# Kernel tuning notes

Hardware: AMD Instinct MI355X
Metric: run time of the kernel (lower is better)

The kernel has to match this reference:

```python
import jax, jax.numpy as jnp
import numpy as np

B, T, D = 2, 2048, 1024
QH, KVH = 16, 4
HD = D // QH          # 64
G = QH // KVH         # group size 4
SCALE = HD ** -0.5


def _rope_rotate(x):
    # interleaved rotation: (x1, x2) -> (-x2, x1)
    x1 = x[..., ::2]
    x2 = x[..., 1::2]
    return jnp.stack((-x2, x1), axis=-1).reshape(x.shape)


def setup_inputs() -> dict:
    key = jax.random.key(0)
    k0, k1, k2, k3 = jax.random.split(key, 4)
    x = jax.random.normal(k0, (B, T, D), dtype=jnp.float32)
    # proper RoPE tables, shape [T, HD], each frequency repeated for the interleaved pair
    inv_freq = 1.0 / (10000.0 ** (np.arange(0, HD, 2, dtype=np.float32) / HD))
    freqs = np.arange(T, dtype=np.float32)[:, None] * inv_freq[None, :]   # [T, HD/2]
    freqs = np.repeat(freqs, 2, axis=-1)                                   # [T, HD]
    cos = jnp.asarray(np.cos(freqs), dtype=jnp.float32)
    sin = jnp.asarray(np.sin(freqs), dtype=jnp.float32)
    # glorot-uniform weights stored torch-style as [out, in]
    def glorot(k, out_d, in_d):
        lim = float(np.sqrt(6.0 / (in_d + out_d)))
        return jax.random.uniform(k, (out_d, in_d), jnp.float32, -lim, lim)
    Wq = glorot(k1, D, D)
    Wkv = glorot(k2, 2 * KVH * HD, D)
    Wo = glorot(k3, D, D)
    return {"x": x, "cos": cos, "sin": sin, "Wq": Wq, "Wkv": Wkv, "Wo": Wo}


def reference(x, cos, sin, Wq, Wkv, Wo):
    # projections (torch Linear: y = x @ W.T)
    q = (x @ Wq.T).reshape(B, T, QH, HD).transpose(0, 2, 1, 3)        # [B,QH,T,HD]
    kv = (x @ Wkv.T).reshape(B, T, KVH, 2, HD)
    k = kv[..., 0, :].transpose(0, 2, 1, 3)                            # [B,KVH,T,HD]
    v = kv[..., 1, :].transpose(0, 2, 1, 3)                            # [B,KVH,T,HD]
    # inline RoPE (cos/sin broadcast over batch & heads)
    q = q * cos + _rope_rotate(q) * sin
    k = k * cos + _rope_rotate(k) * sin
    # GQA via broadcast instead of repeat_interleave (same math)
    qg = q.reshape(B, KVH, G, T, HD)
    scores = jnp.einsum('bkgtd,bksd->bkgts', qg, k) * SCALE            # [B,KVH,G,T,T]
    attn = jax.nn.softmax(scores, axis=-1)  # dropout is identity in eval
    out = jnp.einsum('bkgts,bksd->bkgtd', attn, v)                     # [B,KVH,G,T,HD]
    out = out.reshape(B, QH, T, HD).transpose(0, 2, 1, 3).reshape(B, T, D)
    return out @ Wo.T
```

## Files before the change

### kernel.cpp

```cpp
#include <hip/hip_runtime.h>


typedef __bf16 bf16x8 __attribute__((ext_vector_type(8)));
typedef float f32x4 __attribute__((ext_vector_type(4)));
typedef float f32x16 __attribute__((ext_vector_type(16)));
typedef int i32x4 __attribute__((ext_vector_type(4)));
typedef unsigned short ushort4v __attribute__((ext_vector_type(4)));
typedef unsigned short ushort8v __attribute__((ext_vector_type(8)));
typedef unsigned short u16;
typedef unsigned int u32;

#define DEVINL __device__ __forceinline__

DEVINL float bf2f(u16 u) {
  unsigned int x = ((unsigned int)u) << 16;
  return __builtin_bit_cast(float, x);
}
DEVINL u16 f2bf(float f) {
  unsigned int x = __builtin_bit_cast(unsigned int, f);
  x += 0x7fffu + ((x >> 16) & 1u);
  return (u16)(x >> 16);
}
DEVINL float exp2r(float x) {
  float r;
  asm("v_exp_f32 %0, %1" : "=v"(r) : "v"(x));
  return r;
}
DEVINL void gld16(const u16* g, u16* l) {
  __builtin_amdgcn_global_load_lds(
      (const __attribute__((address_space(1))) void*)g,
      (__attribute__((address_space(3))) void*)l, 16, 0, 0);
}

constexpr int Bb = 2, Tt = 2048, Dd = 1024, QH = 16, KVH = 4, HD = 64;
constexpr float SCALE_L2E = 0.125f * 1.44269504088896340736f;
constexpr int KVSZ = 131072;

__global__ void cvt_all(const float* __restrict__ x, const float* __restrict__ Wq,
                        const float* __restrict__ Wkv, const float* __restrict__ Wo,
                        u16* __restrict__ xb, u16* __restrict__ wqkv,
                        u16* __restrict__ wob) {
  int i = blockIdx.x * 256 + threadIdx.x;
  const float* src;
  u16* dst;
  if (i < 1048576) {
    src = x; dst = xb;
  } else if (i < 1310720) {
    src = Wq - (size_t)1048576 * 4; dst = wqkv - (size_t)1048576 * 4;
  } else if (i < 1441792) {
    src = Wkv - (size_t)1310720 * 4; dst = wqkv + (size_t)1024 * 1024 - (size_t)1310720 * 4;
  } else {
    src = Wo - (size_t)1441792 * 4; dst = wob - (size_t)1441792 * 4;
  }
  float4 v = reinterpret_cast<const float4*>(src)[i];
  ushort4v o = {f2bf(v.x), f2bf(v.y), f2bf(v.z), f2bf(v.w)};
  *reinterpret_cast<ushort4v*>(dst + (size_t)i * 4) = o;
}

template <bool OUT_F32, int BNF>
__global__ __launch_bounds__(256) void gemm_bt(const u16* __restrict__ A,
                                               const u16* __restrict__ Bw,
                                               void* __restrict__ Cout, int M, int N, int K) {
  __shared__ alignas(16) u16 lA[128 * 64];
  __shared__ alignas(16) u16 lB[BNF * 32 * 64];
  const int tid = threadIdx.x;
  const int w = tid >> 6, lane = tid & 63;
  const int r16 = lane & 15, g4 = lane >> 4;
  const int row0 = blockIdx.y * 128, col0 = blockIdx.x * (BNF * 32);
  const int sr = tid >> 3, sc = tid & 7;
  const int NT = K >> 6;

  bf16x8 ra[4], rb[BNF];
  f32x4 acc[4][BNF];
#pragma unroll
  for (int i = 0; i < 4; ++i)
#pragma unroll
    for (int j = 0; j < BNF; ++j) acc[i][j] = f32x4{0.f, 0.f, 0.f, 0.f};

  const int wm = (w >> 1) * 64, wn = (w & 1) * (BNF * 8);

#pragma unroll
  for (int i = 0; i < 4; ++i) {
    int r = i * 32 + sr;
    ra[i] = *reinterpret_cast<const bf16x8*>(A + (size_t)(row0 + r) * K + sc * 8);
  }
#pragma unroll
  for (int i = 0; i < BNF; ++i) {
    int r = i * 32 + sr;
    rb[i] = *reinterpret_cast<const bf16x8*>(Bw + (size_t)(col0 + r) * K + sc * 8);
  }

  for (int kt = 0; kt < NT; ++kt) {
    __syncthreads();
#pragma unroll
    for (int i = 0; i < 4; ++i) {
      int r = i * 32 + sr;
      int c = (sc ^ (r & 7)) * 8;
      *reinterpret_cast<bf16x8*>(&lA[r * 64 + c]) = ra[i];
    }
#pragma unroll
    for (int i = 0; i < BNF; ++i) {
      int r = i * 32 + sr;
      int c = (sc ^ (r & 7)) * 8;
      *reinterpret_cast<bf16x8*>(&lB[r * 64 + c]) = rb[i];
    }
    __syncthreads();
    if (kt + 1 < NT) {
      int k0 = (kt + 1) << 6;
#pragma unroll
      for (int i = 0; i < 4; ++i) {
        int r = i * 32 + sr;
        ra[i] = *reinterpret_cast<const bf16x8*>(A + (size_t)(row0 + r) * K + k0 + sc * 8);
      }
#pragma unroll
      for (int i = 0; i < BNF; ++i) {
        int r = i * 32 + sr;
        rb[i] = *reinterpret_cast<const bf16x8*>(Bw + (size_t)(col0 + r) * K + k0 + sc * 8);
      }
    }
#pragma unroll
    for (int kk = 0; kk < 2; ++kk) {
      bf16x8 af[4], bfr[BNF];
#pragma unroll
      for (int mf = 0; mf < 4; ++mf) {
        int r = wm + mf * 16 + r16;
        int c = ((kk * 4 + g4) ^ (r & 7)) * 8;
        af[mf] = *reinterpret_cast<const bf16x8*>(&lA[r * 64 + c]);
      }
#pragma unroll
      for (int nf = 0; nf < BNF; ++nf) {
        int r = wn * 2 + nf * 16 + r16;
        int c = ((kk * 4 + g4) ^ (r & 7)) * 8;
        bfr[nf] = *reinterpret_cast<const bf16x8*>(&lB[r * 64 + c]);
      }
#pragma unroll
      for (int mf = 0; mf < 4; ++mf)
#pragma unroll
        for (int nf = 0; nf < BNF; ++nf)
          acc[mf][nf] =
              __builtin_amdgcn_mfma_f32_16x16x32_bf16(af[mf], bfr[nf], acc[mf][nf], 0, 0, 0);
    }
  }

#pragma unroll
  for (int mf = 0; mf < 4; ++mf)
#pragma unroll
    for (int nf = 0; nf < BNF; ++nf)
#pragma unroll
      for (int r = 0; r < 4; ++r) {
        size_t row = (size_t)(row0 + wm + mf * 16 + g4 * 4 + r);
        size_t col = (size_t)(col0 + wn * 2 + nf * 16 + r16);
        float v = acc[mf][nf][r];
        if (OUT_F32)
          reinterpret_cast<float*>(Cout)[row * N + col] = v;
        else
          reinterpret_cast<u16*>(Cout)[row * N + col] = f2bf(v);
      }
}

__global__ void rope_vt(const u16* __restrict__ P, const float* __restrict__ cosT,
                        const float* __restrict__ sinT, u16* __restrict__ Q,
                        u16* __restrict__ Kc, u16* __restrict__ Vf) {
  __shared__ u16 tile[64][72];
  const int bid = blockIdx.x;
  const int tid = threadIdx.x;
  if (bid < 10240) {
    int idx = bid * 256 + tid;
    int row = idx / 640, p = idx - row * 640;
    int b = row >> 11, t = row & 2047;
    int n, d;
    u16* outp;
    float scl;
    if (p < 512) {
      n = p * 2;
      int h = n >> 6;
      d = n & 63;
      outp = Q + ((size_t)(b * QH + h) * Tt + t) * HD + d;
      scl = SCALE_L2E;
    } else {
      int r2 = p - 512;
      int kvh = r2 >> 5, dp = r2 & 31;
      d = dp * 2;
      n = 1024 + kvh * 128 + d;
      int bh = b * KVH + kvh;
      int kf = d >> 4, h8 = (d >> 3) & 1, j = d & 7;
      outp = Kc + (size_t)bh * KVSZ + ((t >> 5) * 4 + kf) * 512 + (h8 * 32 + (t & 31)) * 8 + j;
      scl = 1.0f;
    }
    unsigned int pv = *reinterpret_cast<const unsigned int*>(P + (size_t)row * 1536 + n);
    float v0 = bf2f((u16)(pv & 0xffffu)), v1 = bf2f((u16)(pv >> 16));
    float c = cosT[t * HD + d], s = sinT[t * HD + d];
    float o0 = (v0 * c - v1 * s) * scl;
    float o1 = (v1 * c + v0 * s) * scl;
    unsigned int ob = (unsigned int)f2bf(o0) | ((unsigned int)f2bf(o1) << 16);
    *reinterpret_cast<unsigned int*>(outp) = ob;
  } else {
    int rem = bid - 10240;
    int bh = rem >> 5, tt = rem & 31;
    int b = bh >> 2, kvh = bh & 3;
    int t0 = tt * 64;
    int colbase = 1024 + kvh * 128 + 64;
#pragma unroll
    for (int j = 0; j < 4; ++j) {
      int rr = j * 16 + (tid >> 4);
      int cc = (tid & 15) * 4;
      *reinterpret_cast<uint2*>(&tile[rr][cc]) =
          *reinterpret_cast<const uint2*>(P + (size_t)(b * Tt + t0 + rr) * 1536 + colbase + cc);
    }
    __syncthreads();
#pragma unroll
    for (int kk = 0; kk < 2; ++kk) {
      int CH = kk * 256 + tid;
      int df = CH >> 8, sbks = (CH >> 6) & 3, h8 = (CH >> 5) & 1, l = CH & 31;
      int d = df * 32 + l;
      int c = (sbks >> 1) * 4 + (sbks & 1) * 2 + h8;
      ushort8v v;
#pragma unroll
      for (int j = 0; j < 8; ++j) v[j] = tile[c * 8 + j][d];
      u16* dst = Vf + (size_t)bh * KVSZ + (((t0 >> 6) * 2 + df) * 4 + sbks) * 512 +
                 (h8 * 32 + l) * 8;
      *reinterpret_cast<ushort8v*>(dst) = v;
    }
  }
}

__global__ __launch_bounds__(512, 4) void attn_fwd10(const u16* __restrict__ Q,
                                                     const u16* __restrict__ Kf,
                                                     const u16* __restrict__ Vf,
                                                     u16* __restrict__ Oa) {
  __shared__ alignas(16) u16 arena[32768];
  const int tid = threadIdx.x;
  const int w = tid >> 6, lane = tid & 63;
  const int g = w & 3, spl = w >> 2;
  const int l31 = lane & 31, hi = lane >> 5;

  const int fid = blockIdx.x;
  const int xcd = fid & 7, idx = fid >> 3;
  const int b = xcd >> 2, kvh = xcd & 3;
  const int h = kvh * 4 + g;
  const int t0 = idx * 32;
  const size_t bh = (size_t)(b * KVH + kvh);

  const int rg = w & 3;
  const int sv = rg & 1, isV = rg >> 1;
  const u16* gsrc = (isV ? Vf : Kf) + bh * KVSZ + sv * 65536 + spl * 2048 + lane * 8;
  const int ldst0 = isV * 16384 + sv * 4096 + spl * 2048;

  const u16* Qh = Q + ((size_t)(b * QH + h) * Tt + t0 + l31) * HD + hi * 8;
  bf16x8 qf[4];
#pragma unroll
  for (int kf = 0; kf < 4; ++kf)
    qf[kf] = *reinterpret_cast<const bf16x8*>(Qh + kf * 16);

  f32x16 oacc[2];
#pragma unroll
  for (int df = 0; df < 2; ++df)
#pragma unroll
    for (int r = 0; r < 16; ++r) oacc[df][r] = 0.f;
  float lp = 0.f;

#pragma unroll
  for (int i = 0; i < 4; ++i) gld16(gsrc + i * 512, &arena[ldst0 + i * 512]);
  __syncthreads();

  int cur = 0;
  for (int it = 0; it < 16; ++it) {
    if (it < 15) {
      const u16* gs = gsrc + (it + 1) * 4096;
      u16* ld = &arena[ldst0 + (cur ^ 1) * 8192];
#pragma unroll
      for (int i = 0; i < 4; ++i) gld16(gs + i * 512, ld + i * 512);
    }
    const int ktb = cur * 8192 + spl * 4096;
    const int vtb = 16384 + cur * 8192 + spl * 4096;

    f32x16 sacc[2];
#pragma unroll
    for (int sb = 0; sb < 2; ++sb) {
      bf16x8 kfr[4];
#pragma unroll
      for (int kf = 0; kf < 4; ++kf)
        kfr[kf] = *reinterpret_cast<const bf16x8*>(&arena[ktb + sb * 2048 + kf * 512 + lane * 8]);
#pragma unroll
      for (int r = 0; r < 16; ++r) sacc[sb][r] = 0.f;
      __builtin_amdgcn_s_setprio(1);
#pragma unroll
      for (int kf = 0; kf < 4; ++kf)
        sacc[sb] = __builtin_amdgcn_mfma_f32_32x32x16_bf16(kfr[kf], qf[kf], sacc[sb], 0, 0, 0);
      __builtin_amdgcn_s_setprio(0);
    }

    float a0 = 0.f, a1 = 0.f, a2 = 0.f, a3 = 0.f;
#pragma unroll
    for (int sb = 0; sb < 2; ++sb)
#pragma unroll
      for (int r = 0; r < 16; r += 4) {
        float e0 = exp2r(sacc[sb][r]);
        float e1 = exp2r(sacc[sb][r + 1]);
        float e2 = exp2r(sacc[sb][r + 2]);
        float e3 = exp2r(sacc[sb][r + 3]);
        sacc[sb][r] = e0; sacc[sb][r + 1] = e1; sacc[sb][r + 2] = e2; sacc[sb][r + 3] = e3;
        a0 += e0; a1 += e1; a2 += e2; a3 += e3;
      }
    lp += (a0 + a1) + (a2 + a3);

    bf16x8 pf[2][2];
#pragma unroll
    for (int sb = 0; sb < 2; ++sb) {
      u32 pw[8];
#pragma unroll
      for (int r2 = 0; r2 < 8; ++r2) {
        u32 o;
        asm("v_cvt_pk_bf16_f32 %0, %1, %2"
            : "=v"(o)
            : "v"(sacc[sb][2 * r2]), "v"(sacc[sb][2 * r2 + 1]));
        pw[r2] = o;
      }
      u32 fw[2][4];
#pragma unroll
      for (int pp = 0; pp < 4; ++pp) {
        int ks = pp >> 1, o = pp & 1;
        u32 a = pw[ks * 4 + o], bq = pw[ks * 4 + o + 2];
        asm("v_permlane32_swap_b32 %0, %1" : "+v"(a), "+v"(bq));
        fw[ks][o] = a;
        fw[ks][o + 2] = bq;
      }
#pragma unroll
      for (int ks = 0; ks < 2; ++ks) {
        i32x4 iv = {(int)fw[ks][0], (int)fw[ks][1], (int)fw[ks][2], (int)fw[ks][3]};
        pf[sb][ks] = __builtin_bit_cast(bf16x8, iv);
      }
    }

    __builtin_amdgcn_s_setprio(1);
#pragma unroll
    for (int df = 0; df < 2; ++df)
#pragma unroll
      for (int sb = 0; sb < 2; ++sb)
#pragma unroll
        for (int ks = 0; ks < 2; ++ks) {
          bf16x8 vfr = *reinterpret_cast<const bf16x8*>(
              &arena[vtb + (df * 4 + sb * 2 + ks) * 512 + lane * 8]);
          oacc[df] = __builtin_amdgcn_mfma_f32_32x32x16_bf16(vfr, pf[sb][ks], oacc[df], 0, 0, 0);
        }
    __builtin_amdgcn_s_setprio(0);

    __syncthreads();
    cur ^= 1;
  }

  lp += __shfl_xor(lp, 32);
  float* cb = reinterpret_cast<float*>(arena) + ((size_t)g * 32 + l31) * 66;
  if (spl == 1) {
#pragma unroll
    for (int df = 0; df < 2; ++df)
#pragma unroll
      for (int r = 0; r < 16; ++r) {
        int d = df * 32 + (r & 3) + 8 * (r >> 2) + 4 * hi;
        cb[d] = oacc[df][r];
      }
    if (hi == 0) cb[64] = lp;
  }
  __syncthreads();
  if (spl == 0) {
    lp += cb[64];
    float linv = 1.0f / lp;
    u16* otg = arena + 17408 + g * 2304;
#pragma unroll
    for (int df = 0; df < 2; ++df)
#pragma unroll
      for (int r = 0; r < 16; ++r) {
        int d = df * 32 + (r & 3) + 8 * (r >> 2) + 4 * hi;
        otg[l31 * 72 + d] = f2bf((oacc[df][r] + cb[d]) * linv);
      }
  }
  __syncthreads();
  if (spl == 0) {
    const u16* otg = arena + 17408 + g * 2304;
    int tr = lane >> 1, dblk = (lane & 1) * 32;
    u16* gdst = Oa + ((size_t)(b * Tt + t0 + tr)) * Dd + h * HD + dblk;
#pragma unroll
    for (int c = 0; c < 4; ++c) {
      ushort8v vv = *reinterpret_cast<const ushort8v*>(&otg[tr * 72 + dblk + c * 8]);
      *reinterpret_cast<ushort8v*>(gdst + c * 8) = vv;
    }
  }
}

extern "C" void kernel_launch(void* const* d_in, const int* in_sizes, int n_in, void* d_out,
                              int out_size, void* d_ws, size_t ws_size, hipStream_t stream) {
  (void)in_sizes; (void)n_in; (void)out_size; (void)ws_size;
  const float* x = (const float*)d_in[0];
  const float* cosT = (const float*)d_in[1];
  const float* sinT = (const float*)d_in[2];
  const float* Wq = (const float*)d_in[3];
  const float* Wkv = (const float*)d_in[4];
  const float* Wo = (const float*)d_in[5];

  char* p = (char*)d_ws;
  u16* xb = (u16*)p;   p += (size_t)4096 * 1024 * 2;
  u16* wqkv = (u16*)p; p += (size_t)1536 * 1024 * 2;
  u16* wob = (u16*)p;  p += (size_t)1024 * 1024 * 2;
  u16* Pbuf = (u16*)p; p += (size_t)4096 * 1536 * 2;
  u16* Qb = (u16*)p;   p += (size_t)Bb * QH * Tt * HD * 2;
  u16* Kbuf = (u16*)p; p += (size_t)Bb * KVH * Tt * HD * 2;
  u16* Vfb = (u16*)p;  p += (size_t)Bb * KVH * HD * Tt * 2;
  u16* Ob = Pbuf;

  cvt_all<<<6656, 256, 0, stream>>>(x, Wq, Wkv, Wo, xb, wqkv, wob);
  gemm_bt<false, 4><<<dim3(12, 32), 256, 0, stream>>>(xb, wqkv, Pbuf, 4096, 1536, 1024);
  rope_vt<<<10496, 256, 0, stream>>>(Pbuf, cosT, sinT, Qb, Kbuf, Vfb);
  attn_fwd10<<<512, 512, 0, stream>>>(Qb, Kbuf, Vfb, Ob);
  gemm_bt<true, 2><<<dim3(16, 32), 256, 0, stream>>>(Ob, wob, d_out, 4096, 1024, 1024);
}
```

Measured before the change: 99.86 us.

## Double-buffer GEMM LDS tiles with direct global-to-LDS loads

The projection GEMM now stages tiles straight from global memory into a double-buffered LDS area through a gld16 helper, with the XOR swizzle moved onto the global address. The old path loaded into registers and then stored to LDS behind two barriers per step. The next tile is prefetched while the current one is computed, leaving one barrier per iteration. The QKV GEMM also switches to a narrower N tile (BNF 4 to 2) with twice the blocks, which raises block count but lowers per-block reuse and doubles LDS use.

```diff
diff --git a/kernel.cpp b/kernel.cpp
--- a/kernel.cpp
+++ b/kernel.cpp
@@ -61,77 +61,56 @@
 __global__ __launch_bounds__(256) void gemm_bt(const u16* __restrict__ A,
                                                const u16* __restrict__ Bw,
                                                void* __restrict__ Cout, int M, int N, int K) {
-  __shared__ alignas(16) u16 lA[128 * 64];
-  __shared__ alignas(16) u16 lB[BNF * 32 * 64];
+  __shared__ alignas(16) u16 lA[2][128 * 64];
+  __shared__ alignas(16) u16 lB[2][BNF * 32 * 64];
   const int tid = threadIdx.x;
   const int w = tid >> 6, lane = tid & 63;
   const int r16 = lane & 15, g4 = lane >> 4;
   const int row0 = blockIdx.y * 128, col0 = blockIdx.x * (BNF * 32);
   const int sr = tid >> 3, sc = tid & 7;
+  const int csw = sc ^ (sr & 7);
   const int NT = K >> 6;
-
-  bf16x8 ra[4], rb[BNF];
+  const int wm = (w >> 1) * 64, wn2 = (w & 1) * (BNF * 16);
+
   f32x4 acc[4][BNF];
 #pragma unroll
   for (int i = 0; i < 4; ++i)
 #pragma unroll
     for (int j = 0; j < BNF; ++j) acc[i][j] = f32x4{0.f, 0.f, 0.f, 0.f};
 
-  const int wm = (w >> 1) * 64, wn = (w & 1) * (BNF * 8);
-
-#pragma unroll
-  for (int i = 0; i < 4; ++i) {
-    int r = i * 32 + sr;
-    ra[i] = *reinterpret_cast<const bf16x8*>(A + (size_t)(row0 + r) * K + sc * 8);
-  }
-#pragma unroll
-  for (int i = 0; i < BNF; ++i) {
-    int r = i * 32 + sr;
-    rb[i] = *reinterpret_cast<const bf16x8*>(Bw + (size_t)(col0 + r) * K + sc * 8);
-  }
-
+  const u16* Abase = A + (size_t)(row0 + sr) * K + csw * 8;
+  const u16* Bbase = Bw + (size_t)(col0 + sr) * K + csw * 8;
+
+  auto stage = [&](int buf, int kt) {
+    const int k0 = kt << 6;
+#pragma unroll
+    for (int i = 0; i < 4; ++i)
+      gld16(Abase + (size_t)(i * 32) * K + k0, &lA[buf][i * 2048 + w * 512]);
+#pragma unroll
+    for (int i = 0; i < BNF; ++i)
+      gld16(Bbase + (size_t)(i * 32) * K + k0, &lB[buf][i * 2048 + w * 512]);
+  };
+
+  stage(0, 0);
+  __syncthreads();
+
+  int cur = 0;
   for (int kt = 0; kt < NT; ++kt) {
-    __syncthreads();
-#pragma unroll
-    for (int i = 0; i < 4; ++i) {
-      int r = i * 32 + sr;
-      int c = (sc ^ (r & 7)) * 8;
-      *reinterpret_cast<bf16x8*>(&lA[r * 64 + c]) = ra[i];
-    }
-#pragma unroll
-    for (int i = 0; i < BNF; ++i) {
-      int r = i * 32 + sr;
-      int c = (sc ^ (r & 7)) * 8;
-      *reinterpret_cast<bf16x8*>(&lB[r * 64 + c]) = rb[i];
-    }
-    __syncthreads();
-    if (kt + 1 < NT) {
-      int k0 = (kt + 1) << 6;
-#pragma unroll
-      for (int i = 0; i < 4; ++i) {
-        int r = i * 32 + sr;
-        ra[i] = *reinterpret_cast<const bf16x8*>(A + (size_t)(row0 + r) * K + k0 + sc * 8);
-      }
-#pragma unroll
-      for (int i = 0; i < BNF; ++i) {
-        int r = i * 32 + sr;
-        rb[i] = *reinterpret_cast<const bf16x8*>(Bw + (size_t)(col0 + r) * K + k0 + sc * 8);
-      }
-    }
+    if (kt + 1 < NT) stage(cur ^ 1, kt + 1);
 #pragma unroll
     for (int kk = 0; kk < 2; ++kk) {
       bf16x8 af[4], bfr[BNF];
 #pragma unroll
       for (int mf = 0; mf < 4; ++mf) {
         int r = wm + mf * 16 + r16;
-        int c = ((kk * 4 + g4) ^ (r & 7)) * 8;
-        af[mf] = *reinterpret_cast<const bf16x8*>(&lA[r * 64 + c]);
+        int c = (kk * 4 + g4) ^ (r & 7);
+        af[mf] = *reinterpret_cast<const bf16x8*>(&lA[cur][r * 64 + c * 8]);
       }
 #pragma unroll
       for (int nf = 0; nf < BNF; ++nf) {
-        int r = wn * 2 + nf * 16 + r16;
-        int c = ((kk * 4 + g4) ^ (r & 7)) * 8;
-        bfr[nf] = *reinterpret_cast<const bf16x8*>(&lB[r * 64 + c]);
+        int r = wn2 + nf * 16 + r16;
+        int c = (kk * 4 + g4) ^ (r & 7);
+        bfr[nf] = *reinterpret_cast<const bf16x8*>(&lB[cur][r * 64 + c * 8]);
       }
 #pragma unroll
       for (int mf = 0; mf < 4; ++mf)
@@ -140,6 +119,8 @@
           acc[mf][nf] =
               __builtin_amdgcn_mfma_f32_16x16x32_bf16(af[mf], bfr[nf], acc[mf][nf], 0, 0, 0);
     }
+    __syncthreads();
+    cur ^= 1;
   }
 
 #pragma unroll
@@ -149,7 +130,7 @@
 #pragma unroll
       for (int r = 0; r < 4; ++r) {
         size_t row = (size_t)(row0 + wm + mf * 16 + g4 * 4 + r);
-        size_t col = (size_t)(col0 + wn * 2 + nf * 16 + r16);
+        size_t col = (size_t)(col0 + wn2 + nf * 16 + r16);
         float v = acc[mf][nf][r];
         if (OUT_F32)
           reinterpret_cast<float*>(Cout)[row * N + col] = v;
@@ -408,7 +389,7 @@
   u16* Ob = Pbuf;
 
   cvt_all<<<6656, 256, 0, stream>>>(x, Wq, Wkv, Wo, xb, wqkv, wob);
-  gemm_bt<false, 4><<<dim3(12, 32), 256, 0, stream>>>(xb, wqkv, Pbuf, 4096, 1536, 1024);
+  gemm_bt<false, 2><<<dim3(24, 32), 256, 0, stream>>>(xb, wqkv, Pbuf, 4096, 1536, 1024);
   rope_vt<<<10496, 256, 0, stream>>>(Pbuf, cosT, sinT, Qb, Kbuf, Vfb);
   attn_fwd10<<<512, 512, 0, stream>>>(Qb, Kbuf, Vfb, Ob);
   gemm_bt<true, 2><<<dim3(16, 32), 256, 0, stream>>>(Ob, wob, d_out, 4096, 1024, 1024);
```

After: 98.76 us. About the same (-1.1%).

## Fuse RoPE and Q/K/V layout scatter into the QKV projection GEMM epilogue

Applied to the files above, without the earlier changes.

Replaces the separate QKV GEMM plus rope_vt kernel with one GEMM whose epilogue applies RoPE, using a lane shuffle to fetch the paired element, and writes Q, K and the transposed V directly in the attention layouts. This drops the Pbuf round trip through global memory and one kernel launch. The N tile shrinks to 64 columns so each block maps to exactly one head. The trade-off is uncoalesced scattered 2-byte stores and per-element cos/sin loads in the epilogue, and less reuse of A per block.

```diff
diff --git a/kernel.cpp b/kernel.cpp
--- a/kernel.cpp
+++ b/kernel.cpp
@@ -57,6 +57,160 @@
   *reinterpret_cast<ushort4v*>(dst + (size_t)i * 4) = o;
 }
 
+
+__global__ __launch_bounds__(256) void gemm_qkv(const u16* __restrict__ A,
+                                                const u16* __restrict__ Bw,
+                                                const float* __restrict__ cosT,
+                                                const float* __restrict__ sinT,
+                                                u16* __restrict__ Qb,
+                                                u16* __restrict__ Kf,
+                                                u16* __restrict__ Vf) {
+  constexpr int K = 1024;
+  __shared__ alignas(16) u16 lA[128 * 64];
+  __shared__ alignas(16) u16 lB[64 * 64];
+  const int tid = threadIdx.x;
+  const int w = tid >> 6, lane = tid & 63;
+  const int r16 = lane & 15, g4 = lane >> 4;
+  const int row0 = blockIdx.y * 128, col0 = blockIdx.x * 64;
+  const int sr = tid >> 3, sc = tid & 7;
+  const int NT = K >> 6;
+
+  bf16x8 ra[4], rb[2];
+  f32x4 acc[4][2];
+#pragma unroll
+  for (int i = 0; i < 4; ++i)
+#pragma unroll
+    for (int j = 0; j < 2; ++j) acc[i][j] = f32x4{0.f, 0.f, 0.f, 0.f};
+
+  const int wm = (w >> 1) * 64, wn2 = (w & 1) * 32;
+
+#pragma unroll
+  for (int i = 0; i < 4; ++i) {
+    int r = i * 32 + sr;
+    ra[i] = *reinterpret_cast<const bf16x8*>(A + (size_t)(row0 + r) * K + sc * 8);
+  }
+#pragma unroll
+  for (int i = 0; i < 2; ++i) {
+    int r = i * 32 + sr;
+    rb[i] = *reinterpret_cast<const bf16x8*>(Bw + (size_t)(col0 + r) * K + sc * 8);
+  }
+
+  for (int kt = 0; kt < NT; ++kt) {
+    __syncthreads();
+#pragma unroll
+    for (int i = 0; i < 4; ++i) {
+      int r = i * 32 + sr;
+      int c = (sc ^ (r & 7)) * 8;
+      *reinterpret_cast<bf16x8*>(&lA[r * 64 + c]) = ra[i];
+    }
+#pragma unroll
+    for (int i = 0; i < 2; ++i) {
+      int r = i * 32 + sr;
+      int c = (sc ^ (r & 7)) * 8;
+      *reinterpret_cast<bf16x8*>(&lB[r * 64 + c]) = rb[i];
+    }
+    __syncthreads();
+    if (kt + 1 < NT) {
+      int k0 = (kt + 1) << 6;
+#pragma unroll
+      for (int i = 0; i < 4; ++i) {
+        int r = i * 32 + sr;
+        ra[i] = *reinterpret_cast<const bf16x8*>(A + (size_t)(row0 + r) * K + k0 + sc * 8);
+      }
+#pragma unroll
+      for (int i = 0; i < 2; ++i) {
+        int r = i * 32 + sr;
+        rb[i] = *reinterpret_cast<const bf16x8*>(Bw + (size_t)(col0 + r) * K + k0 + sc * 8);
+      }
+    }
+#pragma unroll
+    for (int kk = 0; kk < 2; ++kk) {
+      bf16x8 af[4], bfr[2];
+#pragma unroll
+      for (int mf = 0; mf < 4; ++mf) {
+        int r = wm + mf * 16 + r16;
+        int c = ((kk * 4 + g4) ^ (r & 7)) * 8;
+        af[mf] = *reinterpret_cast<const bf16x8*>(&lA[r * 64 + c]);
+      }
+#pragma unroll
+      for (int nf = 0; nf < 2; ++nf) {
+        int r = wn2 + nf * 16 + r16;
+        int c = ((kk * 4 + g4) ^ (r & 7)) * 8;
+        bfr[nf] = *reinterpret_cast<const bf16x8*>(&lB[r * 64 + c]);
+      }
+#pragma unroll
+      for (int mf = 0; mf < 4; ++mf)
+#pragma unroll
+        for (int nf = 0; nf < 2; ++nf)
+          acc[mf][nf] =
+              __builtin_amdgcn_mfma_f32_16x16x32_bf16(af[mf], bfr[nf], acc[mf][nf], 0, 0, 0);
+    }
+  }
+
+  const float psign = (r16 & 1) ? 1.f : -1.f;
+  if (col0 < 1024) {
+    const int hq = col0 >> 6;
+#pragma unroll
+    for (int nf = 0; nf < 2; ++nf) {
+      const int d = wn2 + nf * 16 + r16;
+#pragma unroll
+      for (int mf = 0; mf < 4; ++mf)
+#pragma unroll
+        for (int r = 0; r < 4; ++r) {
+          int bt = row0 + wm + mf * 16 + g4 * 4 + r;
+          int b = bt >> 11, t = bt & 2047;
+          float v = acc[mf][nf][r];
+          float pv = __shfl_xor(v, 1);
+          float c = cosT[t * 64 + d] * SCALE_L2E;
+          float s = sinT[t * 64 + d] * SCALE_L2E;
+          float o = v * c + psign * pv * s;
+          Qb[((size_t)(b * QH + hq) * Tt + t) * HD + d] = f2bf(o);
+        }
+    }
+  } else {
+    const int kvcol = col0 - 1024;
+    const int kvh = kvcol >> 7, isv = (kvcol >> 6) & 1;
+    if (!isv) {
+#pragma unroll
+      for (int nf = 0; nf < 2; ++nf) {
+        const int d = wn2 + nf * 16 + r16;
+        const int kf = d >> 4, h8 = (d >> 3) & 1, j = d & 7;
+#pragma unroll
+        for (int mf = 0; mf < 4; ++mf)
+#pragma unroll
+          for (int r = 0; r < 4; ++r) {
+            int bt = row0 + wm + mf * 16 + g4 * 4 + r;
+            int b = bt >> 11, t = bt & 2047;
+            float v = acc[mf][nf][r];
+            float pv = __shfl_xor(v, 1);
+            float c = cosT[t * 64 + d], s = sinT[t * 64 + d];
+            float o = v * c + psign * pv * s;
+            size_t bh = (size_t)(b * KVH + kvh);
+            Kf[bh * KVSZ + ((t >> 5) * 4 + kf) * 512 + (h8 * 32 + (t & 31)) * 8 + j] = f2bf(o);
+          }
+      }
+    } else {
+#pragma unroll
+      for (int nf = 0; nf < 2; ++nf) {
+        const int d = wn2 + nf * 16 + r16;
+        const int df = d >> 5, l = d & 31;
+#pragma unroll
+        for (int mf = 0; mf < 4; ++mf)
+#pragma unroll
+          for (int r = 0; r < 4; ++r) {
+            int bt = row0 + wm + mf * 16 + g4 * 4 + r;
+            int b = bt >> 11, t = bt & 2047;
+            size_t bh = (size_t)(b * KVH + kvh);
+            size_t addr = bh * KVSZ +
+                          (((t >> 6) * 2 + df) * 4 + ((t >> 4) & 3)) * 512 +
+                          (((t >> 3) & 1) * 32 + l) * 8 + (t & 7);
+            Vf[addr] = f2bf(acc[mf][nf][r]);
+          }
+      }
+    }
+  }
+}
+
 template <bool OUT_F32, int BNF>
 __global__ __launch_bounds__(256) void gemm_bt(const u16* __restrict__ A,
                                                const u16* __restrict__ Bw,
@@ -77,7 +231,7 @@
 #pragma unroll
     for (int j = 0; j < BNF; ++j) acc[i][j] = f32x4{0.f, 0.f, 0.f, 0.f};
 
-  const int wm = (w >> 1) * 64, wn = (w & 1) * (BNF * 8);
+  const int wm = (w >> 1) * 64, wn2 = (w & 1) * (BNF * 16);
 
 #pragma unroll
   for (int i = 0; i < 4; ++i) {
@@ -129,7 +283,7 @@
       }
 #pragma unroll
       for (int nf = 0; nf < BNF; ++nf) {
-        int r = wn * 2 + nf * 16 + r16;
+        int r = wn2 + nf * 16 + r16;
         int c = ((kk * 4 + g4) ^ (r & 7)) * 8;
         bfr[nf] = *reinterpret_cast<const bf16x8*>(&lB[r * 64 + c]);
       }
@@ -149,79 +303,13 @@
 #pragma unroll
       for (int r = 0; r < 4; ++r) {
         size_t row = (size_t)(row0 + wm + mf * 16 + g4 * 4 + r);
-        size_t col = (size_t)(col0 + wn * 2 + nf * 16 + r16);
+        size_t col = (size_t)(col0 + wn2 + nf * 16 + r16);
         float v = acc[mf][nf][r];
         if (OUT_F32)
           reinterpret_cast<float*>(Cout)[row * N + col] = v;
         else
           reinterpret_cast<u16*>(Cout)[row * N + col] = f2bf(v);
       }
-}
-
-__global__ void rope_vt(const u16* __restrict__ P, const float* __restrict__ cosT,
-                        const float* __restrict__ sinT, u16* __restrict__ Q,
-                        u16* __restrict__ Kc, u16* __restrict__ Vf) {
-  __shared__ u16 tile[64][72];
-  const int bid = blockIdx.x;
-  const int tid = threadIdx.x;
-  if (bid < 10240) {
-    int idx = bid * 256 + tid;
-    int row = idx / 640, p = idx - row * 640;
-    int b = row >> 11, t = row & 2047;
-    int n, d;
-    u16* outp;
-    float scl;
-    if (p < 512) {
-      n = p * 2;
-      int h = n >> 6;
-      d = n & 63;
-      outp = Q + ((size_t)(b * QH + h) * Tt + t) * HD + d;
-      scl = SCALE_L2E;
-    } else {
-      int r2 = p - 512;
-      int kvh = r2 >> 5, dp = r2 & 31;
-      d = dp * 2;
-      n = 1024 + kvh * 128 + d;
-      int bh = b * KVH + kvh;
-      int kf = d >> 4, h8 = (d >> 3) & 1, j = d & 7;
-      outp = Kc + (size_t)bh * KVSZ + ((t >> 5) * 4 + kf) * 512 + (h8 * 32 + (t & 31)) * 8 + j;
-      scl = 1.0f;
-    }
-    unsigned int pv = *reinterpret_cast<const unsigned int*>(P + (size_t)row * 1536 + n);
-    float v0 = bf2f((u16)(pv & 0xffffu)), v1 = bf2f((u16)(pv >> 16));
-    float c = cosT[t * HD + d], s = sinT[t * HD + d];
-    float o0 = (v0 * c - v1 * s) * scl;
-    float o1 = (v1 * c + v0 * s) * scl;
-    unsigned int ob = (unsigned int)f2bf(o0) | ((unsigned int)f2bf(o1) << 16);
-    *reinterpret_cast<unsigned int*>(outp) = ob;
-  } else {
-    int rem = bid - 10240;
-    int bh = rem >> 5, tt = rem & 31;
-    int b = bh >> 2, kvh = bh & 3;
-    int t0 = tt * 64;
-    int colbase = 1024 + kvh * 128 + 64;
-#pragma unroll
-    for (int j = 0; j < 4; ++j) {
-      int rr = j * 16 + (tid >> 4);
-      int cc = (tid & 15) * 4;
-      *reinterpret_cast<uint2*>(&tile[rr][cc]) =
-          *reinterpret_cast<const uint2*>(P + (size_t)(b * Tt + t0 + rr) * 1536 + colbase + cc);
-    }
-    __syncthreads();
-#pragma unroll
-    for (int kk = 0; kk < 2; ++kk) {
-      int CH = kk * 256 + tid;
-      int df = CH >> 8, sbks = (CH >> 6) & 3, h8 = (CH >> 5) & 1, l = CH & 31;
-      int d = df * 32 + l;
-      int c = (sbks >> 1) * 4 + (sbks & 1) * 2 + h8;
-      ushort8v v;
-#pragma unroll
-      for (int j = 0; j < 8; ++j) v[j] = tile[c * 8 + j][d];
-      u16* dst = Vf + (size_t)bh * KVSZ + (((t0 >> 6) * 2 + df) * 4 + sbks) * 512 +
-                 (h8 * 32 + l) * 8;
-      *reinterpret_cast<ushort8v*>(dst) = v;
-    }
-  }
 }
 
 __global__ __launch_bounds__(512, 4) void attn_fwd10(const u16* __restrict__ Q,
@@ -408,8 +496,7 @@
   u16* Ob = Pbuf;
 
   cvt_all<<<6656, 256, 0, stream>>>(x, Wq, Wkv, Wo, xb, wqkv, wob);
-  gemm_bt<false, 4><<<dim3(12, 32), 256, 0, stream>>>(xb, wqkv, Pbuf, 4096, 1536, 1024);
-  rope_vt<<<10496, 256, 0, stream>>>(Pbuf, cosT, sinT, Qb, Kbuf, Vfb);
+  gemm_qkv<<<dim3(24, 32), 256, 0, stream>>>(xb, wqkv, cosT, sinT, Qb, Kbuf, Vfb);
   attn_fwd10<<<512, 512, 0, stream>>>(Qb, Kbuf, Vfb, Ob);
   gemm_bt<true, 2><<<dim3(16, 32), 256, 0, stream>>>(Ob, wob, d_out, 4096, 1024, 1024);
 }
```

After: 92.91 us. 1.07x faster.
